# Kernel optimization log

Measured on AMD Instinct MI355X. Metric: run time of the kernel, lower is better.

## Reference

```python
import jax, jax.numpy as jnp
import numpy as np

N_NODES = 50000
N_EDGES = 800000
D_IN = 64
D_OUT = 64


def setup_inputs() -> dict:
    key = jax.random.key(0)
    k1, k2, k3, k4 = jax.random.split(key, 4)
    x = jax.random.normal(k1, (N_NODES, D_IN), dtype=jnp.float32)
    edge_index = jax.random.randint(k2, (2, N_EDGES), 0, N_NODES, dtype=jnp.int64)
    W = jax.random.normal(k3, (D_IN, D_OUT), dtype=jnp.float32) * (1.0 / np.sqrt(D_IN))
    b = jax.random.normal(k4, (D_OUT,), dtype=jnp.float32) * 0.01
    return {"x": x, "edge_index": edge_index, "W": W, "b": b}


def reference(x, edge_index, W, b):
    N = x.shape[0]
    # Add self-loops (PyG GCNConv default add_self_loops=True)
    loop = jnp.arange(N, dtype=edge_index.dtype)
    src = jnp.concatenate([edge_index[0], loop])  # source j
    dst = jnp.concatenate([edge_index[1], loop])  # target i
    # Linear transform first (standard GCNConv: theta then propagate)
    xw = x @ W  # [N, D_OUT]
    # Symmetric degree normalization: deg over targets of (A + I)
    ones = jnp.ones(src.shape[0], dtype=x.dtype)
    deg = jax.ops.segment_sum(ones, dst, num_segments=N)
    dis = jnp.where(deg > 0, jax.lax.rsqrt(jnp.maximum(deg, 1.0)), 0.0)
    norm = dis[src] * dis[dst]  # [E+N]
    # Gather, weight, scatter-add
    msgs = norm[:, None] * xw[src]  # [E+N, D_OUT]
    out = jax.ops.segment_sum(msgs, dst, num_segments=N) + b
    return jax.nn.relu(out)
```

## Files before the change

### kernel.cpp

```cpp
#include <hip/hip_runtime.h>

#define N_NODES 50000
#define N_EDGES 800000
#define D 64
#define FINE_SHIFT 6
#define NBUCK 782
#define CAP 1280
#define EPB 8192
#define NPART 98
#define CSTRIDE 16
#define WS_POISON 0xAAAAAAAAu

typedef _Float16 f16;
typedef __attribute__((ext_vector_type(4))) _Float16 f16x4;
typedef __attribute__((ext_vector_type(8))) _Float16 f16x8;
typedef __attribute__((ext_vector_type(4))) float f32x4;

__global__ __launch_bounds__(1024) void partition_edges(
    const int* __restrict__ src, const int* __restrict__ dst,
    int* __restrict__ cursor, unsigned int* __restrict__ binned,
    const float* __restrict__ W, f16* __restrict__ Wt16)
{
    __shared__ int hist[NBUCK];
    __shared__ int start_s[NBUCK];
    __shared__ int base_s[NBUCK];
    __shared__ unsigned int staged[EPB];

    int tid = threadIdx.x;
    int eb  = blockIdx.x * EPB;
    int total = N_EDGES - eb; if (total > EPB) total = EPB;

    if (blockIdx.x == 0) {
        for (int j = tid; j < 4096; j += 1024) {
            int n = j >> 6, k = j & 63;
            Wt16[j] = (f16)W[k * 64 + n];
        }
    }

    for (int i = tid; i < NBUCK; i += 1024) hist[i] = 0;
    __syncthreads();

    unsigned int rec[8];
    int rank[8];
    int jb = tid * 8;
    if (jb < total) {
        int4 s0 = *(const int4*)&src[eb + jb];
        int4 s1 = *(const int4*)&src[eb + jb + 4];
        int4 d0 = *(const int4*)&dst[eb + jb];
        int4 d1 = *(const int4*)&dst[eb + jb + 4];
        rec[0] = ((unsigned)d0.x << 16) | (unsigned)s0.x;
        rec[1] = ((unsigned)d0.y << 16) | (unsigned)s0.y;
        rec[2] = ((unsigned)d0.z << 16) | (unsigned)s0.z;
        rec[3] = ((unsigned)d0.w << 16) | (unsigned)s0.w;
        rec[4] = ((unsigned)d1.x << 16) | (unsigned)s1.x;
        rec[5] = ((unsigned)d1.y << 16) | (unsigned)s1.y;
        rec[6] = ((unsigned)d1.z << 16) | (unsigned)s1.z;
        rec[7] = ((unsigned)d1.w << 16) | (unsigned)s1.w;
        #pragma unroll
        for (int u = 0; u < 8; ++u)
            rank[u] = atomicAdd(&hist[rec[u] >> (16 + FINE_SHIFT)], 1);
    } else {
        #pragma unroll
        for (int u = 0; u < 8; ++u) rec[u] = 0xFFFFFFFFu;
    }
    __syncthreads();

    if (tid < 64) {
        int b0 = tid * 13;
        int v[13]; int run = 0;
        #pragma unroll
        for (int j = 0; j < 13; ++j) {
            int idx = b0 + j;
            int c = (idx < NBUCK) ? hist[idx] : 0;
            v[j] = run; run += c;
        }
        int s = run;
        #pragma unroll
        for (int off = 1; off < 64; off <<= 1) {
            int t = __shfl_up(s, off);
            if (tid >= off) s += t;
        }
        int excl = s - run;
        #pragma unroll
        for (int j = 0; j < 13; ++j) {
            int idx = b0 + j;
            if (idx < NBUCK) start_s[idx] = excl + v[j];
        }
    }
    __syncthreads();

    for (int i = tid; i < NBUCK; i += 1024) {
        int c = hist[i];
        base_s[i] = c ? (int)((unsigned)atomicAdd(&cursor[i * CSTRIDE], c) - WS_POISON)
                      : 0;
    }
    #pragma unroll
    for (int u = 0; u < 8; ++u) {
        unsigned int v = rec[u];
        if (v != 0xFFFFFFFFu)
            staged[start_s[v >> 22] + rank[u]] = v;
    }
    __syncthreads();

    for (int i = tid; i < total; i += 1024) {
        unsigned int v = staged[i];
        int cb = v >> 22;
        int gp = base_s[cb] + (i - start_s[cb]);
        if ((unsigned)gp < CAP) binned[(size_t)cb * CAP + gp] = v;
    }
}

__global__ __launch_bounds__(256) void xws_fused(
    const int* __restrict__ cursor, const unsigned int* __restrict__ binned,
    const float* __restrict__ x, const f16* __restrict__ Wt16,
    f16* __restrict__ xwsh)
{
    __shared__ f16 WtH[64][72];
    __shared__ f16 park[64][72];
    __shared__ int h[64];

    int bu = blockIdx.x, tid = threadIdx.x;
    int nb = bu * 64;

    if (tid < 64) h[tid] = 0;
    __syncthreads();

    int cnt = (int)((unsigned)cursor[bu * CSTRIDE] - WS_POISON);
    if (cnt < 0) cnt = 0; if (cnt > CAP) cnt = CAP;
    const unsigned int* br = binned + (size_t)bu * CAP;
    for (int i = tid; i < cnt; i += 256)
        atomicAdd(&h[(br[i] >> 16) & 63], 1);

    for (int j = tid; j < 512; j += 256) {
        int row = j >> 3, seg = (j & 7) * 8;
        *(f16x8*)&WtH[row][seg] = *(const f16x8*)&Wt16[row * 64 + seg];
    }
    __syncthreads();

    int wave = tid >> 6, lane = tid & 63;
    int m = lane & 15, q = lane >> 4;

    int ar = nb + wave * 16 + m;
    if (ar >= N_NODES) ar = N_NODES - 1;
    const float4* x4 = (const float4*)x;
    size_t rb = (size_t)ar * 16;
    float4 p0 = x4[rb + q * 2];
    float4 p1 = x4[rb + q * 2 + 1];
    float4 p2 = x4[rb + 8 + q * 2];
    float4 p3 = x4[rb + 8 + q * 2 + 1];
    f16x8 a0 = { (f16)p0.x, (f16)p0.y, (f16)p0.z, (f16)p0.w,
                 (f16)p1.x, (f16)p1.y, (f16)p1.z, (f16)p1.w };
    f16x8 a1 = { (f16)p2.x, (f16)p2.y, (f16)p2.z, (f16)p2.w,
                 (f16)p3.x, (f16)p3.y, (f16)p3.z, (f16)p3.w };

    f32x4 acc[4];
    #pragma unroll
    for (int t = 0; t < 4; ++t) {
        int n0 = t * 16;
        f16x8 b0 = *(const f16x8*)&WtH[n0 + m][q * 8];
        f16x8 b1 = *(const f16x8*)&WtH[n0 + m][32 + q * 8];
        f32x4 z = { 0.f, 0.f, 0.f, 0.f };
        z = __builtin_amdgcn_mfma_f32_16x16x32_f16(a0, b0, z, 0, 0, 0);
        acc[t] = __builtin_amdgcn_mfma_f32_16x16x32_f16(a1, b1, z, 0, 0, 0);
    }

    float disr[4];
    #pragma unroll
    for (int r = 0; r < 4; ++r)
        disr[r] = rsqrtf((float)h[wave * 16 + q * 4 + r] + 1.0f);
    #pragma unroll
    for (int t = 0; t < 4; ++t) {
        int n0 = t * 16;
        #pragma unroll
        for (int r = 0; r < 4; ++r)
            park[wave * 16 + q * 4 + r][n0 + m] = (f16)(acc[t][r] * disr[r]);
    }
    __syncthreads();

    for (int j = tid; j < 512; j += 256) {
        int row = j >> 3, seg = (j & 7) * 8;
        if (nb + row < N_NODES)
            *(f16x8*)&xwsh[(size_t)(nb + row) * D + seg] = *(const f16x8*)&park[row][seg];
    }
}

__global__ __launch_bounds__(512) void gather_out(
    const int* __restrict__ cursor, const unsigned int* __restrict__ binned,
    const f16* __restrict__ xwsh, const float* __restrict__ b,
    float* __restrict__ out)
{
    __shared__ unsigned short ssrc[CAP];
    __shared__ int h[64], off_s[64], cur[64];

    int cb = blockIdx.x, tid = threadIdx.x;
    int wave = tid >> 6, lane = tid & 63;
    int nb = cb * 64;
    int cnt = (int)((unsigned)cursor[cb * CSTRIDE] - WS_POISON);
    if (cnt < 0) cnt = 0; if (cnt > CAP) cnt = CAP;
    const unsigned int* br = binned + (size_t)cb * CAP;

    if (tid < 64) h[tid] = 0;
    __syncthreads();

    unsigned int rec[3];
    #pragma unroll
    for (int u = 0; u < 3; ++u) {
        int j = u * 512 + tid;
        if (j < cnt) {
            rec[u] = br[j];
            atomicAdd(&h[(rec[u] >> 16) & 63], 1);
        } else rec[u] = 0xFFFFFFFFu;
    }
    __syncthreads();

    if (tid < 64) {
        int v = h[tid], s = v;
        #pragma unroll
        for (int off = 1; off < 64; off <<= 1) {
            int t = __shfl_up(s, off);
            if (tid >= off) s += t;
        }
        off_s[tid] = s - v;
        cur[tid]   = s - v;
    }
    __syncthreads();

    #pragma unroll
    for (int u = 0; u < 3; ++u) {
        unsigned int v = rec[u];
        if (v != 0xFFFFFFFFu) {
            int p = atomicAdd(&cur[(v >> 16) & 63], 1);
            ssrc[p] = (unsigned short)(v & 0xFFFFu);
        }
    }
    __syncthreads();

    const f16x4* xw4 = (const f16x4*)xwsh;
    const float4* b4p = (const float4*)b;
    float4* out4 = (float4*)out;
    int g = lane >> 4, c16 = lane & 15;

    for (int i = 0; i < 8; ++i) {
        int nl = wave * 8 + i;
        int n  = nb + nl;
        if (n >= N_NODES) break;
        int off = off_s[nl], c = h[nl];

        float a0 = 0.f, a1 = 0.f, a2 = 0.f, a3 = 0.f;
        if (g == 0) {
            f16x4 sv = xw4[(size_t)n * 16 + c16];
            a0 = (float)sv.x; a1 = (float)sv.y; a2 = (float)sv.z; a3 = (float)sv.w;
        }
        int k = off + g, e = off + c;
        for (; k + 4 < e; k += 8) {
            int s0 = ssrc[k], s1 = ssrc[k + 4];
            f16x4 v0 = xw4[(size_t)s0 * 16 + c16];
            f16x4 v1 = xw4[(size_t)s1 * 16 + c16];
            a0 += (float)v0.x + (float)v1.x;
            a1 += (float)v0.y + (float)v1.y;
            a2 += (float)v0.z + (float)v1.z;
            a3 += (float)v0.w + (float)v1.w;
        }
        if (k < e) {
            f16x4 v = xw4[(size_t)ssrc[k] * 16 + c16];
            a0 += (float)v.x; a1 += (float)v.y; a2 += (float)v.z; a3 += (float)v.w;
        }
        a0 += __shfl_xor(a0, 32); a1 += __shfl_xor(a1, 32);
        a2 += __shfl_xor(a2, 32); a3 += __shfl_xor(a3, 32);
        a0 += __shfl_xor(a0, 16); a1 += __shfl_xor(a1, 16);
        a2 += __shfl_xor(a2, 16); a3 += __shfl_xor(a3, 16);
        if (g == 0) {
            float dn = rsqrtf((float)c + 1.0f);
            float4 bl = b4p[c16];
            float4 r;
            r.x = fmaxf(bl.x + dn * a0, 0.f);
            r.y = fmaxf(bl.y + dn * a1, 0.f);
            r.z = fmaxf(bl.z + dn * a2, 0.f);
            r.w = fmaxf(bl.w + dn * a3, 0.f);
            out4[(size_t)n * 16 + c16] = r;
        }
    }
}

extern "C" void kernel_launch(void* const* d_in, const int* in_sizes, int n_in,
                              void* d_out, int out_size, void* d_ws, size_t ws_size,
                              hipStream_t stream) {
    const float* x  = (const float*)d_in[0];
    const int*   ei = (const int*)d_in[1];
    const float* W  = (const float*)d_in[2];
    const float* b  = (const float*)d_in[3];

    const int* src = ei;
    const int* dst = ei + N_EDGES;
    float* out = (float*)d_out;

    f16*          xwsh   = (f16*)d_ws;
    int*          cursor = (int*)(xwsh + (size_t)N_NODES * D);
    unsigned int* binned = (unsigned int*)(cursor + NBUCK * CSTRIDE);
    f16*          Wt16   = (f16*)(binned + (size_t)NBUCK * CAP);

    partition_edges<<<NPART, 1024, 0, stream>>>(src, dst, cursor, binned, W, Wt16);
    xws_fused<<<NBUCK, 256, 0, stream>>>(cursor, binned, x, Wt16, xwsh);
    gather_out<<<NBUCK, 512, 0, stream>>>(cursor, binned, xwsh, b, out);
}
```

Measured before the change: 107.0 us.

## Run x@W matmul concurrently with edge partitioning and apply source norm in gather

Extra blocks in the partition kernel now compute the unscaled x@W product in fp16, so the matmul runs alongside edge binning instead of in a separate kernel that had to wait for degrees. A light degree kernel writes per-node rsqrt(deg) to the workspace, and the gather kernel applies the source normalisation per edge via an extra dis[src] load and FMA. The matmul overlaps with partitioning, at the cost of an extra scattered 4-byte load per edge in gather and a union shared-memory buffer that may change partition occupancy.

```diff
diff --git a/kernel.cpp b/kernel.cpp
--- a/kernel.cpp
+++ b/kernel.cpp
@@ -8,6 +8,7 @@
 #define CAP 1280
 #define EPB 8192
 #define NPART 98
+#define NMM 196
 #define CSTRIDE 16
 #define WS_POISON 0xAAAAAAAAu
 
@@ -16,26 +17,80 @@
 typedef __attribute__((ext_vector_type(8))) _Float16 f16x8;
 typedef __attribute__((ext_vector_type(4))) float f32x4;
 
-__global__ __launch_bounds__(1024) void partition_edges(
+#define SMEM_PART (3 * NBUCK * 4 + EPB * 4)
+#define SMEM_MM   (64 * 72 * 2 + 256 * 72 * 2)
+#define SMEM_SZ   (SMEM_MM > SMEM_PART ? SMEM_MM : SMEM_PART)
+
+__global__ __launch_bounds__(1024) void partition_matmul(
     const int* __restrict__ src, const int* __restrict__ dst,
     int* __restrict__ cursor, unsigned int* __restrict__ binned,
-    const float* __restrict__ W, f16* __restrict__ Wt16)
+    const float* __restrict__ W, const float* __restrict__ x,
+    f16* __restrict__ xwh)
 {
-    __shared__ int hist[NBUCK];
-    __shared__ int start_s[NBUCK];
-    __shared__ int base_s[NBUCK];
-    __shared__ unsigned int staged[EPB];
-
+    __shared__ __align__(16) unsigned char smem[SMEM_SZ];
     int tid = threadIdx.x;
+
+    if (blockIdx.x >= NPART) {
+        f16 (*WtH)[72]  = (f16 (*)[72])smem;
+        f16 (*park)[72] = (f16 (*)[72])(smem + 64 * 72 * 2);
+
+        for (int j = tid; j < 4096; j += 1024)
+            WtH[j & 63][j >> 6] = (f16)W[j];
+        __syncthreads();
+
+        int nb = (blockIdx.x - NPART) * 256;
+        int wave = tid >> 6, lane = tid & 63;
+        int m = lane & 15, q = lane >> 4;
+
+        int ar = nb + wave * 16 + m;
+        if (ar >= N_NODES) ar = N_NODES - 1;
+        const float4* x4 = (const float4*)x;
+        size_t rb = (size_t)ar * 16;
+        float4 p0 = x4[rb + q * 2];
+        float4 p1 = x4[rb + q * 2 + 1];
+        float4 p2 = x4[rb + 8 + q * 2];
+        float4 p3 = x4[rb + 8 + q * 2 + 1];
+        f16x8 a0 = { (f16)p0.x, (f16)p0.y, (f16)p0.z, (f16)p0.w,
+                     (f16)p1.x, (f16)p1.y, (f16)p1.z, (f16)p1.w };
+        f16x8 a1 = { (f16)p2.x, (f16)p2.y, (f16)p2.z, (f16)p2.w,
+                     (f16)p3.x, (f16)p3.y, (f16)p3.z, (f16)p3.w };
+
+        f32x4 acc[4];
+        #pragma unroll
+        for (int t = 0; t < 4; ++t) {
+            int n0 = t * 16;
+            f16x8 b0 = *(const f16x8*)&WtH[n0 + m][q * 8];
+            f16x8 b1 = *(const f16x8*)&WtH[n0 + m][32 + q * 8];
+            f32x4 z = { 0.f, 0.f, 0.f, 0.f };
+            z = __builtin_amdgcn_mfma_f32_16x16x32_f16(a0, b0, z, 0, 0, 0);
+            acc[t] = __builtin_amdgcn_mfma_f32_16x16x32_f16(a1, b1, z, 0, 0, 0);
+        }
+
+        #pragma unroll
+        for (int t = 0; t < 4; ++t) {
+            int n0 = t * 16;
+            #pragma unroll
+            for (int r = 0; r < 4; ++r)
+                park[wave * 16 + q * 4 + r][n0 + m] = (f16)acc[t][r];
+        }
+        __syncthreads();
+
+        for (int j = tid; j < 2048; j += 1024) {
+            int row = j >> 3, seg = (j & 7) * 8;
+            int n = nb + row;
+            if (n < N_NODES)
+                *(f16x8*)&xwh[(size_t)n * D + seg] = *(const f16x8*)&park[row][seg];
+        }
+        return;
+    }
+
+    int* hist            = (int*)smem;
+    int* start_s         = hist + NBUCK;
+    int* base_s          = start_s + NBUCK;
+    unsigned int* staged = (unsigned int*)(base_s + NBUCK);
+
     int eb  = blockIdx.x * EPB;
     int total = N_EDGES - eb; if (total > EPB) total = EPB;
-
-    if (blockIdx.x == 0) {
-        for (int j = tid; j < 4096; j += 1024) {
-            int n = j >> 6, k = j & 63;
-            Wt16[j] = (f16)W[k * 64 + n];
-        }
-    }
 
     for (int i = tid; i < NBUCK; i += 1024) hist[i] = 0;
     __syncthreads();
@@ -110,17 +165,12 @@
     }
 }
 
-__global__ __launch_bounds__(256) void xws_fused(
+__global__ __launch_bounds__(256) void degree_dis(
     const int* __restrict__ cursor, const unsigned int* __restrict__ binned,
-    const float* __restrict__ x, const f16* __restrict__ Wt16,
-    f16* __restrict__ xwsh)
+    float* __restrict__ dis)
 {
-    __shared__ f16 WtH[64][72];
-    __shared__ f16 park[64][72];
     __shared__ int h[64];
-
     int bu = blockIdx.x, tid = threadIdx.x;
-    int nb = bu * 64;
 
     if (tid < 64) h[tid] = 0;
     __syncthreads();
@@ -130,64 +180,17 @@
     const unsigned int* br = binned + (size_t)bu * CAP;
     for (int i = tid; i < cnt; i += 256)
         atomicAdd(&h[(br[i] >> 16) & 63], 1);
-
-    for (int j = tid; j < 512; j += 256) {
-        int row = j >> 3, seg = (j & 7) * 8;
-        *(f16x8*)&WtH[row][seg] = *(const f16x8*)&Wt16[row * 64 + seg];
-    }
-    __syncthreads();
-
-    int wave = tid >> 6, lane = tid & 63;
-    int m = lane & 15, q = lane >> 4;
-
-    int ar = nb + wave * 16 + m;
-    if (ar >= N_NODES) ar = N_NODES - 1;
-    const float4* x4 = (const float4*)x;
-    size_t rb = (size_t)ar * 16;
-    float4 p0 = x4[rb + q * 2];
-    float4 p1 = x4[rb + q * 2 + 1];
-    float4 p2 = x4[rb + 8 + q * 2];
-    float4 p3 = x4[rb + 8 + q * 2 + 1];
-    f16x8 a0 = { (f16)p0.x, (f16)p0.y, (f16)p0.z, (f16)p0.w,
-                 (f16)p1.x, (f16)p1.y, (f16)p1.z, (f16)p1.w };
-    f16x8 a1 = { (f16)p2.x, (f16)p2.y, (f16)p2.z, (f16)p2.w,
-                 (f16)p3.x, (f16)p3.y, (f16)p3.z, (f16)p3.w };
-
-    f32x4 acc[4];
-    #pragma unroll
-    for (int t = 0; t < 4; ++t) {
-        int n0 = t * 16;
-        f16x8 b0 = *(const f16x8*)&WtH[n0 + m][q * 8];
-        f16x8 b1 = *(const f16x8*)&WtH[n0 + m][32 + q * 8];
-        f32x4 z = { 0.f, 0.f, 0.f, 0.f };
-        z = __builtin_amdgcn_mfma_f32_16x16x32_f16(a0, b0, z, 0, 0, 0);
-        acc[t] = __builtin_amdgcn_mfma_f32_16x16x32_f16(a1, b1, z, 0, 0, 0);
-    }
-
-    float disr[4];
-    #pragma unroll
-    for (int r = 0; r < 4; ++r)
-        disr[r] = rsqrtf((float)h[wave * 16 + q * 4 + r] + 1.0f);
-    #pragma unroll
-    for (int t = 0; t < 4; ++t) {
-        int n0 = t * 16;
-        #pragma unroll
-        for (int r = 0; r < 4; ++r)
-            park[wave * 16 + q * 4 + r][n0 + m] = (f16)(acc[t][r] * disr[r]);
-    }
-    __syncthreads();
-
-    for (int j = tid; j < 512; j += 256) {
-        int row = j >> 3, seg = (j & 7) * 8;
-        if (nb + row < N_NODES)
-            *(f16x8*)&xwsh[(size_t)(nb + row) * D + seg] = *(const f16x8*)&park[row][seg];
-    }
+    __syncthreads();
+
+    int n = bu * 64 + tid;
+    if (tid < 64 && n < N_NODES)
+        dis[n] = rsqrtf((float)h[tid] + 1.0f);
 }
 
 __global__ __launch_bounds__(512) void gather_out(
     const int* __restrict__ cursor, const unsigned int* __restrict__ binned,
-    const f16* __restrict__ xwsh, const float* __restrict__ b,
-    float* __restrict__ out)
+    const f16* __restrict__ xwh, const float* __restrict__ dis,
+    const float* __restrict__ b, float* __restrict__ out)
 {
     __shared__ unsigned short ssrc[CAP];
     __shared__ int h[64], off_s[64], cur[64];
@@ -235,7 +238,7 @@
     }
     __syncthreads();
 
-    const f16x4* xw4 = (const f16x4*)xwsh;
+    const f16x4* xw4 = (const f16x4*)xwh;
     const float4* b4p = (const float4*)b;
     float4* out4 = (float4*)out;
     int g = lane >> 4, c16 = lane & 15;
@@ -245,32 +248,37 @@
         int n  = nb + nl;
         if (n >= N_NODES) break;
         int off = off_s[nl], c = h[nl];
+        float dn = rsqrtf((float)c + 1.0f);
 
         float a0 = 0.f, a1 = 0.f, a2 = 0.f, a3 = 0.f;
         if (g == 0) {
             f16x4 sv = xw4[(size_t)n * 16 + c16];
-            a0 = (float)sv.x; a1 = (float)sv.y; a2 = (float)sv.z; a3 = (float)sv.w;
+            a0 = dn * (float)sv.x; a1 = dn * (float)sv.y;
+            a2 = dn * (float)sv.z; a3 = dn * (float)sv.w;
         }
         int k = off + g, e = off + c;
         for (; k + 4 < e; k += 8) {
             int s0 = ssrc[k], s1 = ssrc[k + 4];
+            float d0 = dis[s0], d1 = dis[s1];
             f16x4 v0 = xw4[(size_t)s0 * 16 + c16];
             f16x4 v1 = xw4[(size_t)s1 * 16 + c16];
-            a0 += (float)v0.x + (float)v1.x;
-            a1 += (float)v0.y + (float)v1.y;
-            a2 += (float)v0.z + (float)v1.z;
-            a3 += (float)v0.w + (float)v1.w;
+            a0 = fmaf(d0, (float)v0.x, a0); a0 = fmaf(d1, (float)v1.x, a0);
+            a1 = fmaf(d0, (float)v0.y, a1); a1 = fmaf(d1, (float)v1.y, a1);
+            a2 = fmaf(d0, (float)v0.z, a2); a2 = fmaf(d1, (float)v1.z, a2);
+            a3 = fmaf(d0, (float)v0.w, a3); a3 = fmaf(d1, (float)v1.w, a3);
         }
         if (k < e) {
-            f16x4 v = xw4[(size_t)ssrc[k] * 16 + c16];
-            a0 += (float)v.x; a1 += (float)v.y; a2 += (float)v.z; a3 += (float)v.w;
+            int s = ssrc[k];
+            float d = dis[s];
+            f16x4 v = xw4[(size_t)s * 16 + c16];
+            a0 = fmaf(d, (float)v.x, a0); a1 = fmaf(d, (float)v.y, a1);
+            a2 = fmaf(d, (float)v.z, a2); a3 = fmaf(d, (float)v.w, a3);
         }
         a0 += __shfl_xor(a0, 32); a1 += __shfl_xor(a1, 32);
         a2 += __shfl_xor(a2, 32); a3 += __shfl_xor(a3, 32);
         a0 += __shfl_xor(a0, 16); a1 += __shfl_xor(a1, 16);
         a2 += __shfl_xor(a2, 16); a3 += __shfl_xor(a3, 16);
         if (g == 0) {
-            float dn = rsqrtf((float)c + 1.0f);
             float4 bl = b4p[c16];
             float4 r;
             r.x = fmaxf(bl.x + dn * a0, 0.f);
@@ -294,12 +302,12 @@
     const int* dst = ei + N_EDGES;
     float* out = (float*)d_out;
 
-    f16*          xwsh   = (f16*)d_ws;
-    int*          cursor = (int*)(xwsh + (size_t)N_NODES * D);
+    f16*          xwh    = (f16*)d_ws;
+    int*          cursor = (int*)(xwh + (size_t)N_NODES * D);
     unsigned int* binned = (unsigned int*)(cursor + NBUCK * CSTRIDE);
-    f16*          Wt16   = (f16*)(binned + (size_t)NBUCK * CAP);
-
-    partition_edges<<<NPART, 1024, 0, stream>>>(src, dst, cursor, binned, W, Wt16);
-    xws_fused<<<NBUCK, 256, 0, stream>>>(cursor, binned, x, Wt16, xwsh);
-    gather_out<<<NBUCK, 512, 0, stream>>>(cursor, binned, xwsh, b, out);
+    float*        dis    = (float*)(binned + (size_t)NBUCK * CAP);
+
+    partition_matmul<<<NPART + NMM, 1024, 0, stream>>>(src, dst, cursor, binned, W, x, xwh);
+    degree_dis<<<NBUCK, 256, 0, stream>>>(cursor, binned, dis);
+    gather_out<<<NBUCK, 512, 0, stream>>>(cursor, binned, xwh, dis, b, out);
 }
```

New measurement: 105.8 us. No clear change (-1.2%).
